# Performance work log

Measured on AMD Instinct MI355X. Metric: run time of the kernel, lower is better.

Reference implementation:

```python
import jax, jax.numpy as jnp
import numpy as np
import math

D = 2048
H = 8
DK = D // H // 2  # 128
NL = 3
EPS = 1e-6
SCALE = 1.0 / math.sqrt(DK)


def _ln(x, g, b):
    m = jnp.mean(x, axis=-1, keepdims=True)
    v = jnp.mean(jnp.square(x - m), axis=-1, keepdims=True)
    return (x - m) * jax.lax.rsqrt(v + EPS) * g + b


def _attn_layer(x, g, b, Wq, Wk, Wv):
    bs = x.shape[0]
    xn = _ln(x, g, b)
    # torch Linear: y = x @ W.T ; reshape to (bs, h, 2, d_k)
    q = (xn @ Wq.T).reshape(bs, H, 2, DK)
    k = (xn @ Wk.T).reshape(bs, H, 2, DK)
    v = (xn @ Wv.T).reshape(bs, H, 2, DK)
    s = jnp.einsum('bhpd,bhqd->bhpq', q, k) * SCALE  # tiny 2x2 scores
    a = jax.nn.softmax(s, axis=-1)
    o = jnp.einsum('bhpq,bhqd->bhpd', a, v).reshape(bs, D)
    return o + x


def _ff_layer(x, lnd_g, lnd_b, lnt_g, lnt_b, Wd1, bd1, Wd2, bd2, Wt1, bt1, Wt2, bt2):
    d, t = x[:, :D // 2], x[:, D // 2:]
    dn = _ln(d, lnd_g, lnd_b)
    tn = _ln(t, lnt_g, lnt_b)
    do = jax.nn.relu(dn @ Wd1.T + bd1) @ Wd2.T + bd2
    to = jax.nn.relu(tn @ Wt1.T + bt1) @ Wt2.T + bt2
    return jnp.concatenate([do, to], axis=-1) + x


def setup_inputs() -> dict:
    key = jax.random.key(0)
    ks = iter(jax.random.split(key, 64))
    s = 0.02
    inp = {}
    inp['x'] = jax.random.normal(next(ks), (8192, D), dtype=jnp.float32)
    # attention stacks: NL layers
    inp['attn_ln_g'] = jnp.ones((NL, D), jnp.float32)
    inp['attn_ln_b'] = jnp.zeros((NL, D), jnp.float32)
    inp['Wq'] = jax.random.normal(next(ks), (NL, D, D), jnp.float32) * s
    inp['Wk'] = jax.random.normal(next(ks), (NL, D, D), jnp.float32) * s
    inp['Wv'] = jax.random.normal(next(ks), (NL, D, D), jnp.float32) * s
    # feedforward stacks: NL-1 layers
    F = NL - 1
    hd = D // 2
    inp['ff_lnd_g'] = jnp.ones((F, hd), jnp.float32)
    inp['ff_lnd_b'] = jnp.zeros((F, hd), jnp.float32)
    inp['ff_lnt_g'] = jnp.ones((F, hd), jnp.float32)
    inp['ff_lnt_b'] = jnp.zeros((F, hd), jnp.float32)
    inp['Wd1'] = jax.random.normal(next(ks), (F, D, hd), jnp.float32) * s
    inp['bd1'] = jnp.zeros((F, D), jnp.float32)
    inp['Wd2'] = jax.random.normal(next(ks), (F, hd, D), jnp.float32) * s
    inp['bd2'] = jnp.zeros((F, hd), jnp.float32)
    inp['Wt1'] = jax.random.normal(next(ks), (F, D, hd), jnp.float32) * s
    inp['bt1'] = jnp.zeros((F, D), jnp.float32)
    inp['Wt2'] = jax.random.normal(next(ks), (F, hd, D), jnp.float32) * s
    inp['bt2'] = jnp.zeros((F, hd), jnp.float32)
    # output head
    inp['Wo1'] = jax.random.normal(next(ks), (hd, D), jnp.float32) * s
    inp['bo1'] = jnp.zeros((hd,), jnp.float32)
    inp['Wo2'] = jax.random.normal(next(ks), (1, hd), jnp.float32) * s
    inp['bo2'] = jnp.zeros((1,), jnp.float32)
    return inp


def reference(x, attn_ln_g, attn_ln_b, Wq, Wk, Wv,
              ff_lnd_g, ff_lnd_b, ff_lnt_g, ff_lnt_b,
              Wd1, bd1, Wd2, bd2, Wt1, bt1, Wt2, bt2,
              Wo1, bo1, Wo2, bo2):
    for n in range(NL - 1):
        x = _attn_layer(x, attn_ln_g[n], attn_ln_b[n], Wq[n], Wk[n], Wv[n])
        x = _ff_layer(x, ff_lnd_g[n], ff_lnd_b[n], ff_lnt_g[n], ff_lnt_b[n],
                      Wd1[n], bd1[n], Wd2[n], bd2[n], Wt1[n], bt1[n], Wt2[n], bt2[n])
    x = _attn_layer(x, attn_ln_g[-1], attn_ln_b[-1], Wq[-1], Wk[-1], Wv[-1])
    h = jax.nn.relu(x @ Wo1.T + bo1)
    return h @ Wo2.T + bo2  # [bs, 1]
```

## Files before the change

### kernel.cpp

```cpp
#include <hip/hip_runtime.h>
#include <stdint.h>


typedef __bf16 bf16x8 __attribute__((ext_vector_type(8)));
typedef float f32x4 __attribute__((ext_vector_type(4)));

static __device__ __forceinline__ float bf2f(unsigned short u) {
  unsigned int x = ((unsigned int)u) << 16;
  float f;
  __builtin_memcpy(&f, &x, 4);
  return f;
}
static __device__ __forceinline__ unsigned short f2bf(float f) {
  unsigned int x;
  __builtin_memcpy(&x, &f, 4);
  x += 0x7fffu + ((x >> 16) & 1u);
  return (unsigned short)(x >> 16);
}

static __device__ __forceinline__ void gload_lds16(const void* g, void* l) {
  __builtin_amdgcn_global_load_lds(
      (const __attribute__((address_space(1))) unsigned int*)g,
      (__attribute__((address_space(3))) unsigned int*)l, 16, 0, 0);
}

__global__ __launch_bounds__(256) void cvt_kernel(
    const float* __restrict__ in, unsigned short* __restrict__ out, long n) {
  const long i = ((long)blockIdx.x * 256 + threadIdx.x) * 4;
  if (i + 3 < n) {
    float4 f = *(const float4*)(in + i);
    *(ushort4*)(out + i) = make_ushort4(f2bf(f.x), f2bf(f.y), f2bf(f.z), f2bf(f.w));
  }
}

#define BARRIER __builtin_amdgcn_s_barrier()
#define LGKM(N)                                                     \
  do {                                                              \
    asm volatile("s_waitcnt lgkmcnt(" #N ")" ::: "memory");         \
    __builtin_amdgcn_sched_barrier(0);                              \
  } while (0)
#define VMC(N)                                                      \
  do {                                                              \
    asm volatile("s_waitcnt vmcnt(" #N ")" ::: "memory");           \
    __builtin_amdgcn_sched_barrier(0);                              \
  } while (0)

__global__ __launch_bounds__(512, 2) void gemm8_kernel(
    const unsigned short* __restrict__ A, int lda,
    const unsigned short* __restrict__ B, int K,
    void* __restrict__ Cp, int ldc, const float* __restrict__ bias,
    int relu, int out_f32, int resadd,
    const unsigned short* __restrict__ A2, const unsigned short* __restrict__ B2,
    void* __restrict__ C2p, const float* __restrict__ bias2, int dual) {
  extern __shared__ __align__(16) char smem[];

  const int tid = threadIdx.x;
  const int lane = tid & 63;
  const int w = tid >> 6;
  const int wm = w >> 2;
  const int wn = w & 3;
  const long brow = (long)blockIdx.y * 256;

  const unsigned short* Ap = A;
  const unsigned short* Bp = B;
  const float* bi = bias;
  void* Cq = Cp;
  long bcol;
  if (dual && (int)blockIdx.x >= (int)(gridDim.x >> 1)) {
    Ap = A2; Bp = B2; bi = bias2; Cq = C2p;
    bcol = (long)(blockIdx.x - (gridDim.x >> 1)) * 256;
  } else {
    bcol = (long)blockIdx.x * 256;
  }

  const int NT = K >> 6;

  const int lrA = tid >> 3;
  const int scb = ((tid & 7) * 16) ^ (((tid >> 3) & 7) << 4);
  const unsigned wb = (unsigned)(tid & ~63) * 16;
  const long ldab = (long)lda * 2;
  const long ldbb = (long)K * 2;
  const char* gA = (const char*)Ap + (brow + lrA) * ldab + scb;
  const char* gB = (const char*)Bp + (bcol + lrA) * ldbb + scb;
  const long a64 = 64 * ldab, a128 = 128 * ldab, a192 = 192 * ldab;
  const long b64 = 64 * ldbb, b128 = 128 * ldbb, b192 = 192 * ldbb;

#define STAGE_A(bb, off)                                        \
  do {                                                          \
    gload_lds16(gA + (off), smem + (bb) + wb);                  \
    gload_lds16(gA + a64 + (off), smem + (bb) + 8192 + wb);     \
    gload_lds16(gA + a128 + (off), smem + (bb) + 16384 + wb);   \
    gload_lds16(gA + a192 + (off), smem + (bb) + 24576 + wb);   \
  } while (0)
#define STAGE_B(bb, off)                                        \
  do {                                                          \
    gload_lds16(gB + (off), smem + (bb) + 32768 + wb);          \
    gload_lds16(gB + b64 + (off), smem + (bb) + 40960 + wb);    \
    gload_lds16(gB + b128 + (off), smem + (bb) + 49152 + wb);   \
    gload_lds16(gB + b192 + (off), smem + (bb) + 57344 + wb);   \
  } while (0)

  f32x4 acc[8][4];
  const f32x4 fz = {0.f, 0.f, 0.f, 0.f};
#pragma unroll
  for (int m = 0; m < 8; ++m)
#pragma unroll
    for (int n = 0; n < 4; ++n) acc[m][n] = fz;

  const int frow = lane & 15;
  const int fkb = (lane >> 4) * 16;
  const int fswz = (lane & 7) << 4;

#define RDA(dst, CB, M, KK)                                                   \
  dst = *(const bf16x8*)(smem + (CB) + (wm * 128 + (M) * 16 + frow) * 128 +   \
                         (((KK) * 64 + fkb) ^ fswz))
#define RDB(dst, CB, N, KK)                                                   \
  dst = *(const bf16x8*)(smem + (CB) + 32768 +                                \
                         (wn * 64 + (N) * 16 + frow) * 128 +                  \
                         (((KK) * 64 + fkb) ^ fswz))

#define MM8(AF, MA, BF, NA, MO, NO)                                           \
  do {                                                                        \
    _Pragma("unroll") for (int kk = 0; kk < 2; ++kk)                          \
    _Pragma("unroll") for (int mm = 0; mm < 2; ++mm)                          \
    _Pragma("unroll") for (int nn = 0; nn < 2; ++nn)                          \
        acc[(MO) + mm][(NO) + nn] = __builtin_amdgcn_mfma_f32_16x16x32_bf16(  \
            AF[(MA) + mm][kk], BF[(NA) + nn][kk], acc[(MO) + mm][(NO) + nn],  \
            0, 0, 0);                                                         \
  } while (0)
#define MM8N(AF, BF, NB, NO)                                                  \
  do {                                                                        \
    _Pragma("unroll") for (int kk = 0; kk < 2; ++kk)                          \
    _Pragma("unroll") for (int mm = 0; mm < 4; ++mm)                          \
        acc[mm][(NO)] = __builtin_amdgcn_mfma_f32_16x16x32_bf16(              \
            AF[mm][kk], BF[(NB)][kk], acc[mm][(NO)], 0, 0, 0);                \
  } while (0)

  bf16x8 afL[4][2], afH[4][2], bfvL[2][2], bfvH[2][2];

  STAGE_A(0, 0);
  STAGE_B(0, 0);
  STAGE_A(65536, 128);
  STAGE_B(65536, 128);
  VMC(8);
  BARRIER;
  long soff = 256;

#define TILE_IT(T, CB)                                                        \
  do {                                                                        \
                                       \
    RDB(bfvL[0][0], CB, 0, 0); RDB(bfvL[0][1], CB, 0, 1);                     \
    RDB(bfvL[1][0], CB, 1, 0); RDB(bfvL[1][1], CB, 1, 1);                     \
    RDA(afL[0][0], CB, 0, 0); RDA(afL[0][1], CB, 0, 1);                       \
    RDA(afL[1][0], CB, 1, 0); RDA(afL[1][1], CB, 1, 1);                       \
    RDA(afL[2][0], CB, 2, 0); RDA(afL[2][1], CB, 2, 1);                       \
    RDA(afL[3][0], CB, 3, 0); RDA(afL[3][1], CB, 3, 1);                       \
    BARRIER;                                                                  \
    LGKM(4);                                                                  \
    __builtin_amdgcn_s_setprio(1);                                            \
    MM8(afL, 0, bfvL, 0, 0, 0);                                               \
    LGKM(0);                                                                  \
    MM8(afL, 2, bfvL, 0, 2, 0);                                               \
    __builtin_amdgcn_s_setprio(0);                                            \
    BARRIER;                                                                  \
                                              \
    RDB(bfvH[0][0], CB, 2, 0); RDB(bfvH[0][1], CB, 2, 1);                     \
    RDB(bfvH[1][0], CB, 3, 0); RDB(bfvH[1][1], CB, 3, 1);                     \
    BARRIER;                                                                  \
    LGKM(2);                                                                  \
    __builtin_amdgcn_s_setprio(1);                                            \
    MM8N(afL, bfvH, 0, 2);                                                    \
    LGKM(0);                                                                  \
    MM8N(afL, bfvH, 1, 3);                                                    \
    __builtin_amdgcn_s_setprio(0);                                            \
    BARRIER;                                                                  \
                                \
    RDA(afH[0][0], CB, 4, 0); RDA(afH[0][1], CB, 4, 1);                       \
    RDA(afH[1][0], CB, 5, 0); RDA(afH[1][1], CB, 5, 1);                       \
    RDA(afH[2][0], CB, 6, 0); RDA(afH[2][1], CB, 6, 1);                       \
    RDA(afH[3][0], CB, 7, 0); RDA(afH[3][1], CB, 7, 1);                       \
    if ((T) + 2 < NT) STAGE_B(CB, soff);                                      \
    BARRIER;                                                                  \
    LGKM(4);                                                                  \
    __builtin_amdgcn_s_setprio(1);                                            \
    MM8(afH, 0, bfvL, 0, 4, 0);                                               \
    LGKM(0);                                                                  \
    MM8(afH, 2, bfvL, 0, 6, 0);                                               \
    __builtin_amdgcn_s_setprio(0);                                            \
    BARRIER;                                                                  \
                                \
    if ((T) + 2 < NT) {                                                       \
      STAGE_A(CB, soff);                                                      \
      VMC(8);                                                                 \
    } else {                                                                  \
      VMC(0);                                                                 \
    }                                                                         \
    BARRIER;                                                                  \
    __builtin_amdgcn_s_setprio(1);                                            \
    MM8(afH, 0, bfvH, 0, 4, 2);                                               \
    MM8(afH, 2, bfvH, 0, 6, 2);                                               \
    __builtin_amdgcn_s_setprio(0);                                            \
    BARRIER;                                                                  \
    soff += 128;                                                              \
  } while (0)

  for (int t = 0; t < NT; t += 2) {
    TILE_IT(t, 0);
    TILE_IT(t + 1, 65536);
  }

  const long rb0 = brow + wm * 128 + (lane >> 4) * 4;
  const long cb0 = bcol + wn * 64 + (lane & 15);
#pragma unroll
  for (int m = 0; m < 8; ++m) {
#pragma unroll
    for (int n = 0; n < 4; ++n) {
      const long col = cb0 + n * 16;
      const float bv = bi ? bi[col] : 0.f;
#pragma unroll
      for (int j = 0; j < 4; ++j) {
        const long r = rb0 + m * 16 + j;
        float v = acc[m][n][j] + bv;
        if (relu) v = fmaxf(v, 0.f);
        if (out_f32) {
          float* cp = (float*)Cq + r * (long)ldc + col;
          if (resadd) v += *cp;
          *cp = v;
        } else {
          ((unsigned short*)Cq)[r * (long)ldc + col] = f2bf(v);
        }
      }
    }
  }
#undef TILE_IT
#undef STAGE_A
#undef STAGE_B
#undef RDA
#undef RDB
#undef MM8
#undef MM8N
}

__global__ __launch_bounds__(256) void gemm_bt_kernel(
    const unsigned short* __restrict__ A, int lda,
    const unsigned short* __restrict__ B, int K,
    void* __restrict__ Cp, int ldc,
    const float* __restrict__ bias,
    const void* __restrict__ res, int res_mode, int ldres,
    int relu, int out_f32) {
  __shared__ __align__(16) unsigned short As[128 * 32];
  __shared__ __align__(16) unsigned short Bs[128 * 32];

  const int t = threadIdx.x;
  const int lane = t & 63;
  const int w = t >> 6;
  const int wr = (w >> 1) * 64;
  const int wc = (w & 1) * 64;
  const long brow = (long)blockIdx.y * 128;
  const long bcol = (long)blockIdx.x * 128;

  const int srow = lane >> 2;
  const int scol = (lane & 3) * 8;
  const unsigned short* Ab = A + (brow + w * 32 + srow) * (long)lda + scol;
  const unsigned short* Bb = B + (bcol + w * 32 + srow) * (long)K + scol;
  unsigned short* Asb = &As[(w * 32) * 32];
  unsigned short* Bsb = &Bs[(w * 32) * 32];

  f32x4 acc[4][4];
  const f32x4 fzero = {0.f, 0.f, 0.f, 0.f};
#pragma unroll
  for (int m = 0; m < 4; ++m)
#pragma unroll
    for (int n = 0; n < 4; ++n) acc[m][n] = fzero;

  const int fr = lane & 15;
  const int fk = (lane >> 4) * 8;

  for (int kt = 0; kt < K; kt += 32) {
    gload_lds16(Ab + kt, Asb);
    gload_lds16(Ab + 16 * (long)lda + kt, Asb + 16 * 32);
    gload_lds16(Bb + kt, Bsb);
    gload_lds16(Bb + 16 * (long)K + kt, Bsb + 16 * 32);
    __syncthreads();

    bf16x8 af[4], bfv[4];
#pragma unroll
    for (int m = 0; m < 4; ++m)
      af[m] = *(const bf16x8*)&As[(wr + m * 16 + fr) * 32 + fk];
#pragma unroll
    for (int n = 0; n < 4; ++n)
      bfv[n] = *(const bf16x8*)&Bs[(wc + n * 16 + fr) * 32 + fk];
#pragma unroll
    for (int m = 0; m < 4; ++m)
#pragma unroll
      for (int n = 0; n < 4; ++n)
        acc[m][n] = __builtin_amdgcn_mfma_f32_16x16x32_bf16(af[m], bfv[n],
                                                            acc[m][n], 0, 0, 0);
    __syncthreads();
  }

  const long rbase = brow + wr + (lane >> 4) * 4;
#pragma unroll
  for (int m = 0; m < 4; ++m) {
#pragma unroll
    for (int n = 0; n < 4; ++n) {
      const long col = bcol + wc + n * 16 + fr;
      const float bv = bias ? bias[col] : 0.f;
#pragma unroll
      for (int j = 0; j < 4; ++j) {
        const long r = rbase + m * 16 + j;
        float v = acc[m][n][j] + bv;
        if (relu) v = fmaxf(v, 0.f);
        if (res_mode == 1)
          v += ((const float*)res)[r * (long)ldres + col];
        else if (res_mode == 2)
          v += bf2f(((const unsigned short*)res)[r * (long)ldres + col]);
        if (out_f32)
          ((float*)Cp)[r * (long)ldc + col] = v;
        else
          ((unsigned short*)Cp)[r * (long)ldc + col] = f2bf(v);
      }
    }
  }
}

template <int L>
__global__ __launch_bounds__(256) void ln_kernel(
    const void* __restrict__ inp, int in_bf16, int ldin,
    const float* __restrict__ g, const float* __restrict__ b,
    unsigned short* __restrict__ outp, int ldout) {
  constexpr int VEC = L / 256;
  const long row = blockIdx.x;
  const int t = threadIdx.x;
  float v[VEC];
  if (in_bf16) {
    const unsigned short* p = (const unsigned short*)inp + row * (long)ldin + t * VEC;
#pragma unroll
    for (int i = 0; i < VEC; i += 4) {
      ushort4 u = *(const ushort4*)(p + i);
      v[i] = bf2f(u.x); v[i + 1] = bf2f(u.y); v[i + 2] = bf2f(u.z); v[i + 3] = bf2f(u.w);
    }
  } else {
    const float* p = (const float*)inp + row * (long)ldin + t * VEC;
#pragma unroll
    for (int i = 0; i < VEC; i += 4) {
      float4 f = *(const float4*)(p + i);
      v[i] = f.x; v[i + 1] = f.y; v[i + 2] = f.z; v[i + 3] = f.w;
    }
  }
  float s = 0.f, sq = 0.f;
#pragma unroll
  for (int i = 0; i < VEC; ++i) { s += v[i]; sq += v[i] * v[i]; }
#pragma unroll
  for (int off = 32; off; off >>= 1) {
    s += __shfl_xor(s, off, 64);
    sq += __shfl_xor(sq, off, 64);
  }
  __shared__ float red[8];
  if ((t & 63) == 0) { red[t >> 6] = s; red[4 + (t >> 6)] = sq; }
  __syncthreads();
  s = red[0] + red[1] + red[2] + red[3];
  sq = red[4] + red[5] + red[6] + red[7];
  const float mean = s * (1.f / L);
  const float var = sq * (1.f / L) - mean * mean;
  const float rstd = rsqrtf(var + 1e-6f);
  unsigned short* op = outp + row * (long)ldout + t * VEC;
  const float* gp = g + t * VEC;
  const float* bp = b + t * VEC;
#pragma unroll
  for (int i = 0; i < VEC; i += 4) {
    float4 gg = *(const float4*)(gp + i);
    float4 bb = *(const float4*)(bp + i);
    *(ushort4*)(op + i) = make_ushort4(
        f2bf((v[i + 0] - mean) * rstd * gg.x + bb.x),
        f2bf((v[i + 1] - mean) * rstd * gg.y + bb.y),
        f2bf((v[i + 2] - mean) * rstd * gg.z + bb.z),
        f2bf((v[i + 3] - mean) * rstd * gg.w + bb.w));
  }
}

__global__ __launch_bounds__(512) void attn_glue_kernel(
    const unsigned short* __restrict__ Q, const unsigned short* __restrict__ Kq,
    const unsigned short* __restrict__ V, int ld, const void* __restrict__ Xres,
    int res_bf16, void* __restrict__ Xout, int out_bf16,
    unsigned short* __restrict__ Xout_bf,
    unsigned short* __restrict__ DNp, unsigned short* __restrict__ TNp,
    const float* __restrict__ lnd_g, const float* __restrict__ lnd_b,
    const float* __restrict__ lnt_g, const float* __restrict__ lnt_b) {
  const long row = blockIdx.x;
  const int h = threadIdx.x >> 6;
  const int lane = threadIdx.x & 63;
  const long qbase = row * (long)ld + h * 256;
  const long xbase = row * 2048 + h * 256;
  const int d = lane * 2;

  ushort2 q0 = *(const ushort2*)&Q[qbase + d];
  ushort2 q1 = *(const ushort2*)&Q[qbase + 128 + d];
  ushort2 k0 = *(const ushort2*)&Kq[qbase + d];
  ushort2 k1 = *(const ushort2*)&Kq[qbase + 128 + d];
  ushort2 v0 = *(const ushort2*)&V[qbase + d];
  ushort2 v1 = *(const ushort2*)&V[qbase + 128 + d];

  const float q0x = bf2f(q0.x), q0y = bf2f(q0.y);
  const float q1x = bf2f(q1.x), q1y = bf2f(q1.y);
  const float k0x = bf2f(k0.x), k0y = bf2f(k0.y);
  const float k1x = bf2f(k1.x), k1y = bf2f(k1.y);

  float s00 = q0x * k0x + q0y * k0y;
  float s01 = q0x * k1x + q0y * k1y;
  float s10 = q1x * k0x + q1y * k0y;
  float s11 = q1x * k1x + q1y * k1y;
#pragma unroll
  for (int off = 32; off; off >>= 1) {
    s00 += __shfl_xor(s00, off, 64);
    s01 += __shfl_xor(s01, off, 64);
    s10 += __shfl_xor(s10, off, 64);
    s11 += __shfl_xor(s11, off, 64);
  }
  const float SC = 0.088388347648318447f;
  s00 *= SC; s01 *= SC; s10 *= SC; s11 *= SC;
  const float m0 = fmaxf(s00, s01), m1 = fmaxf(s10, s11);
  const float e00 = __expf(s00 - m0), e01 = __expf(s01 - m0);
  const float e10 = __expf(s10 - m1), e11 = __expf(s11 - m1);
  const float i0 = 1.f / (e00 + e01), i1 = 1.f / (e10 + e11);
  const float a00 = e00 * i0, a01 = e01 * i0;
  const float a10 = e10 * i1, a11 = e11 * i1;

  const float v0x = bf2f(v0.x), v0y = bf2f(v0.y);
  const float v1x = bf2f(v1.x), v1y = bf2f(v1.y);
  float o0x = a00 * v0x + a01 * v1x, o0y = a00 * v0y + a01 * v1y;
  float o1x = a10 * v0x + a11 * v1x, o1y = a10 * v0y + a11 * v1y;

  if (res_bf16) {
    const unsigned short* xr = (const unsigned short*)Xres + xbase;
    ushort2 ra = *(const ushort2*)&xr[d];
    ushort2 rb = *(const ushort2*)&xr[128 + d];
    o0x += bf2f(ra.x); o0y += bf2f(ra.y); o1x += bf2f(rb.x); o1y += bf2f(rb.y);
  } else {
    const float* xr = (const float*)Xres + xbase;
    float2 ra = *(const float2*)&xr[d];
    float2 rb = *(const float2*)&xr[128 + d];
    o0x += ra.x; o0y += ra.y; o1x += rb.x; o1y += rb.y;
  }
  if (out_bf16) {
    unsigned short* xo = (unsigned short*)Xout + xbase;
    *(ushort2*)&xo[d] = make_ushort2(f2bf(o0x), f2bf(o0y));
    *(ushort2*)&xo[128 + d] = make_ushort2(f2bf(o1x), f2bf(o1y));
  } else {
    float* xo = (float*)Xout + xbase;
    *(float2*)&xo[d] = make_float2(o0x, o0y);
    *(float2*)&xo[128 + d] = make_float2(o1x, o1y);
  }
  if (Xout_bf) {
    unsigned short* xb = Xout_bf + xbase;
    *(ushort2*)&xb[d] = make_ushort2(f2bf(o0x), f2bf(o0y));
    *(ushort2*)&xb[128 + d] = make_ushort2(f2bf(o1x), f2bf(o1y));
  }

  if (DNp) {
    float s4 = o0x + o0y + o1x + o1y;
    float q4 = o0x * o0x + o0y * o0y + o1x * o1x + o1y * o1y;
#pragma unroll
    for (int off = 32; off; off >>= 1) {
      s4 += __shfl_xor(s4, off, 64);
      q4 += __shfl_xor(q4, off, 64);
    }
    __shared__ float redS[8], redQ[8];
    if (lane == 0) { redS[h] = s4; redQ[h] = q4; }
    __syncthreads();
    const int b4 = (h >> 2) * 4;
    const float S = redS[b4] + redS[b4 + 1] + redS[b4 + 2] + redS[b4 + 3];
    const float Qs = redQ[b4] + redQ[b4 + 1] + redQ[b4 + 2] + redQ[b4 + 3];
    const float mean = S * (1.f / 1024.f);
    const float var = Qs * (1.f / 1024.f) - mean * mean;
    const float rstd = rsqrtf(var + 1e-6f);
    const float* gp = (h < 4) ? lnd_g : lnt_g;
    const float* bp = (h < 4) ? lnd_b : lnt_b;
    unsigned short* dst = ((h < 4) ? DNp : TNp) + row * 1024;
    const int hc = (h & 3) * 256 + d;
    float2 g0 = *(const float2*)&gp[hc];
    float2 b0 = *(const float2*)&bp[hc];
    *(ushort2*)&dst[hc] = make_ushort2(f2bf((o0x - mean) * rstd * g0.x + b0.x),
                                       f2bf((o0y - mean) * rstd * g0.y + b0.y));
    float2 g1 = *(const float2*)&gp[hc + 128];
    float2 b1 = *(const float2*)&bp[hc + 128];
    *(ushort2*)&dst[hc + 128] =
        make_ushort2(f2bf((o1x - mean) * rstd * g1.x + b1.x),
                     f2bf((o1y - mean) * rstd * g1.y + b1.y));
  }
}

__global__ __launch_bounds__(256) void final_matvec_kernel(
    const unsigned short* __restrict__ Hm, const float* __restrict__ wv,
    const float* __restrict__ b2, float* __restrict__ outp) {
  const long row = blockIdx.x;
  const int t = threadIdx.x;
  ushort4 hv = *(const ushort4*)&Hm[row * 1024 + t * 4];
  float4 wq = *(const float4*)&wv[t * 4];
  float s = bf2f(hv.x) * wq.x + bf2f(hv.y) * wq.y +
            bf2f(hv.z) * wq.z + bf2f(hv.w) * wq.w;
#pragma unroll
  for (int off = 32; off; off >>= 1) s += __shfl_xor(s, off, 64);
  __shared__ float red[4];
  if ((t & 63) == 0) red[t >> 6] = s;
  __syncthreads();
  if (t == 0) outp[row] = red[0] + red[1] + red[2] + red[3] + b2[0];
}

extern "C" void kernel_launch(void* const* d_in, const int* in_sizes, int n_in,
                              void* d_out, int out_size, void* d_ws,
                              size_t ws_size, hipStream_t stream) {
  const float* x_in = (const float*)d_in[0];
  const float* aln_g = (const float*)d_in[1];
  const float* aln_b = (const float*)d_in[2];
  const float* Wq_f = (const float*)d_in[3];
  const float* Wk_f = (const float*)d_in[4];
  const float* Wv_f = (const float*)d_in[5];
  const float* lnd_g = (const float*)d_in[6];
  const float* lnd_b = (const float*)d_in[7];
  const float* lnt_g = (const float*)d_in[8];
  const float* lnt_b = (const float*)d_in[9];
  const float* Wd1_f = (const float*)d_in[10];
  const float* bd1 = (const float*)d_in[11];
  const float* Wd2_f = (const float*)d_in[12];
  const float* bd2 = (const float*)d_in[13];
  const float* Wt1_f = (const float*)d_in[14];
  const float* bt1 = (const float*)d_in[15];
  const float* Wt2_f = (const float*)d_in[16];
  const float* bt2 = (const float*)d_in[17];
  const float* Wo1_f = (const float*)d_in[18];
  const float* bo1 = (const float*)d_in[19];
  const float* Wo2_f = (const float*)d_in[20];
  const float* bo2 = (const float*)d_in[21];

  const size_t R = 8192, D = 2048, HD = 1024;
  const size_t DD = D * D;
  const size_t WALL = (3 * 3 * DD + 4 * 2 * D * HD + HD * D) * 2;
  const size_t SLOT = 3 * DD * 2;
  const size_t ACT = R * D * 4 + R * D * 2 + R * 6144 * 2;

  auto cvt = [&](const float* src, unsigned short* dst, long n) {
    cvt_kernel<<<dim3((unsigned)(n / 1024)), dim3(256), 0, stream>>>(src, dst, n);
  };

  if (ws_size >= ACT + SLOT) {
    const bool planAll = ws_size >= ACT + WALL;
    hipFuncSetAttribute(reinterpret_cast<const void*>(gemm8_kernel),
                        hipFuncAttributeMaxDynamicSharedMemorySize, 131072);

    char* p = (char*)d_ws;
    float* Xf = (float*)p; p += R * D * 4;
    unsigned short* XN = (unsigned short*)p; p += R * D * 2;
    unsigned short* QKVb = (unsigned short*)p; p += R * 6144 * 2;
    unsigned short* Warea = (unsigned short*)p;

    unsigned short* H1d = QKVb;
    unsigned short* H1t = QKVb + R * 2048;
    unsigned short* Hfin = QKVb + R * 4096;
    unsigned short* DN = XN;
    unsigned short* TN = XN + R * HD;

    unsigned short* Wqkv_b = Warea;
    unsigned short* Wd1_b = Wqkv_b + 9 * DD;
    unsigned short* Wt1_b = Wd1_b + 2 * D * HD;
    unsigned short* Wd2_b = Wt1_b + 2 * D * HD;
    unsigned short* Wt2_b = Wd2_b + 2 * D * HD;
    unsigned short* Wo1_b = Wt2_b + 2 * D * HD;
    if (planAll) {
      for (int n = 0; n < 3; ++n) {
        cvt(Wq_f + n * DD, Wqkv_b + n * 3 * DD + 0 * DD, DD);
        cvt(Wk_f + n * DD, Wqkv_b + n * 3 * DD + 1 * DD, DD);
        cvt(Wv_f + n * DD, Wqkv_b + n * 3 * DD + 2 * DD, DD);
      }
      cvt(Wd1_f, Wd1_b, 2 * D * HD);
      cvt(Wt1_f, Wt1_b, 2 * D * HD);
      cvt(Wd2_f, Wd2_b, 2 * D * HD);
      cvt(Wt2_f, Wt2_b, 2 * D * HD);
      cvt(Wo1_f, Wo1_b, HD * D);
    }

    auto gemm8 = [&](const unsigned short* A, int lda, const unsigned short* B,
                     int N, int K, void* C, int ldc, const float* bias,
                     int relu, int of32, int resadd, const unsigned short* A2,
                     const unsigned short* B2, void* C2, const float* bias2) {
      const int dual = (A2 != nullptr);
      dim3 grid((dual ? 2 : 1) * (N / 256), 32);
      gemm8_kernel<<<grid, dim3(512), 131072, stream>>>(
          A, lda, B, K, C, ldc, bias, relu, of32, resadd, A2, B2, C2, bias2,
          dual);
    };

    for (int n = 0; n < 3; ++n) {
      ln_kernel<2048><<<8192, 256, 0, stream>>>(
          (n == 0) ? (const void*)x_in : (const void*)Xf, 0, 2048,
          aln_g + n * D, aln_b + n * D, XN, 2048);
      const unsigned short* Wqkv;
      if (planAll) {
        Wqkv = Wqkv_b + (size_t)n * 3 * DD;
      } else {
        cvt(Wq_f + n * DD, Warea + 0 * DD, DD);
        cvt(Wk_f + n * DD, Warea + 1 * DD, DD);
        cvt(Wv_f + n * DD, Warea + 2 * DD, DD);
        Wqkv = Warea;
      }
      gemm8(XN, 2048, Wqkv, 6144, 2048, QKVb, 6144, nullptr, 0, 0, 0,
            nullptr, nullptr, nullptr, nullptr);
      attn_glue_kernel<<<8192, 512, 0, stream>>>(
          QKVb, QKVb + 2048, QKVb + 4096, 6144,
          (n == 0) ? (const void*)x_in : (const void*)Xf, 0, Xf, 0,
          (n == 2) ? XN : nullptr,
          (n < 2) ? DN : nullptr, (n < 2) ? TN : nullptr,
          (n < 2) ? lnd_g + n * HD : nullptr, (n < 2) ? lnd_b + n * HD : nullptr,
          (n < 2) ? lnt_g + n * HD : nullptr, (n < 2) ? lnt_b + n * HD : nullptr);

      if (n < 2) {
        const size_t fo = (size_t)n * D * HD;
        const unsigned short *w1d, *w1t, *w2d, *w2t;
        if (planAll) {
          w1d = Wd1_b + fo; w1t = Wt1_b + fo; w2d = Wd2_b + fo; w2t = Wt2_b + fo;
        } else {
          cvt(Wd1_f + fo, Warea + 0 * D * HD, D * HD);
          cvt(Wt1_f + fo, Warea + 1 * D * HD, D * HD);
          cvt(Wd2_f + fo, Warea + 2 * D * HD, D * HD);
          cvt(Wt2_f + fo, Warea + 3 * D * HD, D * HD);
          w1d = Warea; w1t = Warea + D * HD; w2d = Warea + 2 * D * HD;
          w2t = Warea + 3 * D * HD;
        }
        gemm8(DN, 1024, w1d, 2048, 1024, H1d, 2048, bd1 + n * D, 1, 0, 0,
              TN, w1t, H1t, bt1 + n * D);
        gemm8(H1d, 2048, w2d, 1024, 2048, Xf, 2048, bd2 + n * HD, 0, 1, 1,
              H1t, w2t, Xf + HD, bt2 + n * HD);
      }
    }

    const unsigned short* Wo1p;
    if (planAll) {
      Wo1p = Wo1_b;
    } else {
      cvt(Wo1_f, Warea, HD * D);
      Wo1p = Warea;
    }
    gemm8(XN, 2048, Wo1p, 1024, 2048, Hfin, 1024, bo1, 1, 0, 0,
          nullptr, nullptr, nullptr, nullptr);
    final_matvec_kernel<<<8192, 256, 0, stream>>>(Hfin, Wo2_f, bo2,
                                                  (float*)d_out);
    return;
  }

  const size_t PLB = R * D * 2;
  const size_t XFZ = R * D * 4;
  const size_t SLOT1 = DD * 2;
  const bool planAll = ws_size >= XFZ + 4 * PLB + WALL;
  const bool xIsF32 = planAll || ws_size >= XFZ + 4 * PLB + SLOT1;

  char* p = (char*)d_ws;
  float* Xf = nullptr;
  unsigned short* Xb = nullptr;
  if (xIsF32) { Xf = (float*)p; p += XFZ; } else { Xb = (unsigned short*)p; p += PLB; }
  unsigned short* XN = (unsigned short*)p; p += PLB;
  unsigned short* Qb = (unsigned short*)p; p += PLB;
  unsigned short* Kb = (unsigned short*)p; p += PLB;
  unsigned short* Vb = (unsigned short*)p; p += PLB;
  unsigned short* Warea = (unsigned short*)p;

  void* X = xIsF32 ? (void*)Xf : (void*)Xb;
  const int xres_mode = xIsF32 ? 1 : 2;
  unsigned short* H1 = Qb;
  unsigned short* DN = XN;
  unsigned short* TN = XN + R * HD;
  unsigned short* Hfin = Vb;

  unsigned short* Wq_b = Warea;
  unsigned short* Wk_b = Wq_b + 3 * DD;
  unsigned short* Wv_b = Wk_b + 3 * DD;
  unsigned short* Wd1_b = Wv_b + 3 * DD;
  unsigned short* Wd2_b = Wd1_b + 2 * D * HD;
  unsigned short* Wt1_b = Wd2_b + 2 * D * HD;
  unsigned short* Wt2_b = Wt1_b + 2 * D * HD;
  unsigned short* Wo1_b = Wt2_b + 2 * D * HD;
  if (planAll) {
    cvt(Wq_f, Wq_b, 3 * DD);
    cvt(Wk_f, Wk_b, 3 * DD);
    cvt(Wv_f, Wv_b, 3 * DD);
    cvt(Wd1_f, Wd1_b, 2 * D * HD);
    cvt(Wd2_f, Wd2_b, 2 * D * HD);
    cvt(Wt1_f, Wt1_b, 2 * D * HD);
    cvt(Wt2_f, Wt2_b, 2 * D * HD);
    cvt(Wo1_f, Wo1_b, HD * D);
  }
  auto wbf = [&](const float* src_base, unsigned short* pre_base, size_t off,
                 size_t cnt) -> const unsigned short* {
    if (planAll) return pre_base + off;
    cvt(src_base + off, Warea, (long)cnt);
    return Warea;
  };
  auto gemm = [&](const unsigned short* A, int lda, const unsigned short* B,
                  int N, int K, void* C, int ldc, const float* bias,
                  const void* res, int res_mode, int ldres, int relu, int of32) {
    dim3 grid(N / 128, 8192 / 128);
    gemm_bt_kernel<<<grid, dim3(256), 0, stream>>>(
        A, lda, B, K, C, ldc, bias, res, res_mode, ldres, relu, of32);
  };

  for (int n = 0; n < 3; ++n) {
    const void* lin = (n == 0) ? (const void*)x_in : (const void*)X;
    const int lin_bf16 = (n == 0) ? 0 : (xIsF32 ? 0 : 1);
    ln_kernel<2048><<<8192, 256, 0, stream>>>(lin, lin_bf16, 2048,
                                              aln_g + n * D, aln_b + n * D, XN, 2048);
    const size_t wo = (size_t)n * DD;
    gemm(XN, 2048, wbf(Wq_f, Wq_b, wo, DD), 2048, 2048, Qb, 2048,
         nullptr, nullptr, 0, 0, 0, 0);
    gemm(XN, 2048, wbf(Wk_f, Wk_b, wo, DD), 2048, 2048, Kb, 2048,
         nullptr, nullptr, 0, 0, 0, 0);
    gemm(XN, 2048, wbf(Wv_f, Wv_b, wo, DD), 2048, 2048, Vb, 2048,
         nullptr, nullptr, 0, 0, 0, 0);
    attn_glue_kernel<<<8192, 512, 0, stream>>>(
        Qb, Kb, Vb, 2048, (n == 0) ? (const void*)x_in : (const void*)X,
        (n == 0) ? 0 : (xIsF32 ? 0 : 1), X, xIsF32 ? 0 : 1,
        (n == 2 && xIsF32) ? XN : nullptr,
        nullptr, nullptr, nullptr, nullptr, nullptr, nullptr);

    if (n < 2) {
      const size_t fo = (size_t)n * D * HD;
      ln_kernel<1024><<<8192, 256, 0, stream>>>(X, !xIsF32, 2048,
                                                lnd_g + n * HD, lnd_b + n * HD, DN, 1024);
      const void* Xt = xIsF32 ? (const void*)(Xf + HD) : (const void*)(Xb + HD);
      ln_kernel<1024><<<8192, 256, 0, stream>>>(Xt, !xIsF32, 2048,
                                                lnt_g + n * HD, lnt_b + n * HD, TN, 1024);
      void* Xd2 = X;
      void* Xt2 = xIsF32 ? (void*)(Xf + HD) : (void*)(Xb + HD);
      gemm(DN, 1024, wbf(Wd1_f, Wd1_b, fo, D * HD), 2048, 1024, H1, 2048,
           bd1 + n * D, nullptr, 0, 0, 1, 0);
      gemm(H1, 2048, wbf(Wd2_f, Wd2_b, fo, D * HD), 1024, 2048, Xd2, 2048,
           bd2 + n * HD, Xd2, xres_mode, 2048, 0, xIsF32 ? 1 : 0);
      gemm(TN, 1024, wbf(Wt1_f, Wt1_b, fo, D * HD), 2048, 1024, H1, 2048,
           bt1 + n * D, nullptr, 0, 0, 1, 0);
      gemm(H1, 2048, wbf(Wt2_f, Wt2_b, fo, D * HD), 1024, 2048, Xt2, 2048,
           bt2 + n * HD, Xt2, xres_mode, 2048, 0, xIsF32 ? 1 : 0);
    }
  }

  const unsigned short* Afin = xIsF32 ? XN : Xb;
  gemm(Afin, 2048, wbf(Wo1_f, Wo1_b, 0, HD * D), 1024, 2048, Hfin, 1024,
       bo1, nullptr, 0, 0, 1, 0);
  final_matvec_kernel<<<8192, 256, 0, stream>>>(Hfin, Wo2_f, bo2, (float*)d_out);
}
```

Measured before the change: 1.323 ms.

## Remap GEMM workgroups per XCD, batch weight casts, simplify LDS waits, skip dead store

The GEMM kernel now remaps block IDs so each XCD gets a contiguous chunk of output tiles, aiming to improve L2 reuse of A/B panels. The fourteen separate weight-conversion launches are merged into one multi-segment cast kernel to cut launch overhead. The LDS wait counts in the main loop are simplified to full waits before the MFMA groups, which gives up some overlap between LDS reads and math. The last attention layer also skips writing the fp32 residual output, since only the bf16 copy is consumed afterwards.

```diff
diff --git a/kernel.cpp b/kernel.cpp
--- a/kernel.cpp
+++ b/kernel.cpp
@@ -31,6 +31,23 @@
     float4 f = *(const float4*)(in + i);
     *(ushort4*)(out + i) = make_ushort4(f2bf(f.x), f2bf(f.y), f2bf(f.z), f2bf(f.w));
   }
+}
+
+#define MAXSEG 14
+struct CvtArgs {
+  const float* src[MAXSEG];
+  unsigned short* dst[MAXSEG];
+  long pfx[MAXSEG + 1];
+  int ns;
+};
+__global__ __launch_bounds__(256) void cvt_multi_kernel(CvtArgs a) {
+  const long i = ((long)blockIdx.x * 256 + threadIdx.x) * 4;
+  int s = 0;
+  while (s + 1 < a.ns && i >= a.pfx[s + 1]) ++s;
+  const long off = i - a.pfx[s];
+  float4 f = *(const float4*)(a.src[s] + off);
+  *(ushort4*)(a.dst[s] + off) =
+      make_ushort4(f2bf(f.x), f2bf(f.y), f2bf(f.z), f2bf(f.w));
 }
 
 #define BARRIER __builtin_amdgcn_s_barrier()
@@ -59,18 +76,27 @@
   const int w = tid >> 6;
   const int wm = w >> 2;
   const int wn = w & 3;
-  const long brow = (long)blockIdx.y * 256;
+
+  const int gx = (int)gridDim.x;
+  const int nwg = gx * (int)gridDim.y;
+  const int orig = (int)blockIdx.y * gx + (int)blockIdx.x;
+  const int qch = nwg >> 3, rch = nwg & 7, xcd = orig & 7, io = orig >> 3;
+  const int wgid =
+      (xcd < rch ? xcd * (qch + 1) : rch * (qch + 1) + (xcd - rch) * qch) + io;
+  const int bx = wgid % gx;
+  const int by = wgid / gx;
+  const long brow = (long)by * 256;
 
   const unsigned short* Ap = A;
   const unsigned short* Bp = B;
   const float* bi = bias;
   void* Cq = Cp;
   long bcol;
-  if (dual && (int)blockIdx.x >= (int)(gridDim.x >> 1)) {
+  if (dual && bx >= (gx >> 1)) {
     Ap = A2; Bp = B2; bi = bias2; Cq = C2p;
-    bcol = (long)(blockIdx.x - (gridDim.x >> 1)) * 256;
+    bcol = (long)(bx - (gx >> 1)) * 256;
   } else {
-    bcol = (long)blockIdx.x * 256;
+    bcol = (long)bx * 256;
   }
 
   const int NT = K >> 6;
@@ -148,18 +174,18 @@
 
 #define TILE_IT(T, CB)                                                        \
   do {                                                                        \
-                                       \
+                            \
     RDB(bfvL[0][0], CB, 0, 0); RDB(bfvL[0][1], CB, 0, 1);                     \
     RDB(bfvL[1][0], CB, 1, 0); RDB(bfvL[1][1], CB, 1, 1);                     \
     RDA(afL[0][0], CB, 0, 0); RDA(afL[0][1], CB, 0, 1);                       \
     RDA(afL[1][0], CB, 1, 0); RDA(afL[1][1], CB, 1, 1);                       \
     RDA(afL[2][0], CB, 2, 0); RDA(afL[2][1], CB, 2, 1);                       \
     RDA(afL[3][0], CB, 3, 0); RDA(afL[3][1], CB, 3, 1);                       \
+    LGKM(8);                    \
     BARRIER;                                                                  \
-    LGKM(4);                                                                  \
+    LGKM(0);                                                                  \
     __builtin_amdgcn_s_setprio(1);                                            \
     MM8(afL, 0, bfvL, 0, 0, 0);                                               \
-    LGKM(0);                                                                  \
     MM8(afL, 2, bfvL, 0, 2, 0);                                               \
     __builtin_amdgcn_s_setprio(0);                                            \
     BARRIER;                                                                  \
@@ -167,13 +193,13 @@
     RDB(bfvH[0][0], CB, 2, 0); RDB(bfvH[0][1], CB, 2, 1);                     \
     RDB(bfvH[1][0], CB, 3, 0); RDB(bfvH[1][1], CB, 3, 1);                     \
     BARRIER;                                                                  \
-    LGKM(2);                                                                  \
+    LGKM(0);                                                                  \
     __builtin_amdgcn_s_setprio(1);                                            \
     MM8N(afL, bfvH, 0, 2);                                                    \
-    LGKM(0);                                                                  \
     MM8N(afL, bfvH, 1, 3);                                                    \
     __builtin_amdgcn_s_setprio(0);                                            \
     BARRIER;                                                                  \
+                 \
                                 \
     RDA(afH[0][0], CB, 4, 0); RDA(afH[0][1], CB, 4, 1);                       \
     RDA(afH[1][0], CB, 5, 0); RDA(afH[1][1], CB, 5, 1);                       \
@@ -181,19 +207,19 @@
     RDA(afH[3][0], CB, 7, 0); RDA(afH[3][1], CB, 7, 1);                       \
     if ((T) + 2 < NT) STAGE_B(CB, soff);                                      \
     BARRIER;                                                                  \
-    LGKM(4);                                                                  \
+    LGKM(0);                                                                  \
     __builtin_amdgcn_s_setprio(1);                                            \
     MM8(afH, 0, bfvL, 0, 4, 0);                                               \
-    LGKM(0);                                                                  \
     MM8(afH, 2, bfvL, 0, 6, 0);                                               \
     __builtin_amdgcn_s_setprio(0);                                            \
     BARRIER;                                                                  \
+                 \
                                 \
     if ((T) + 2 < NT) {                                                       \
       STAGE_A(CB, soff);                                                      \
-      VMC(8);                                                                 \
+      VMC(8);                                      \
     } else {                                                                  \
-      VMC(0);                                                                 \
+      VMC(0);                                                 \
     }                                                                         \
     BARRIER;                                                                  \
     __builtin_amdgcn_s_setprio(1);                                            \
@@ -442,14 +468,16 @@
     float2 rb = *(const float2*)&xr[128 + d];
     o0x += ra.x; o0y += ra.y; o1x += rb.x; o1y += rb.y;
   }
-  if (out_bf16) {
-    unsigned short* xo = (unsigned short*)Xout + xbase;
-    *(ushort2*)&xo[d] = make_ushort2(f2bf(o0x), f2bf(o0y));
-    *(ushort2*)&xo[128 + d] = make_ushort2(f2bf(o1x), f2bf(o1y));
-  } else {
-    float* xo = (float*)Xout + xbase;
-    *(float2*)&xo[d] = make_float2(o0x, o0y);
-    *(float2*)&xo[128 + d] = make_float2(o1x, o1y);
+  if (Xout) {
+    if (out_bf16) {
+      unsigned short* xo = (unsigned short*)Xout + xbase;
+      *(ushort2*)&xo[d] = make_ushort2(f2bf(o0x), f2bf(o0y));
+      *(ushort2*)&xo[128 + d] = make_ushort2(f2bf(o1x), f2bf(o1y));
+    } else {
+      float* xo = (float*)Xout + xbase;
+      *(float2*)&xo[d] = make_float2(o0x, o0y);
+      *(float2*)&xo[128 + d] = make_float2(o1x, o1y);
+    }
   }
   if (Xout_bf) {
     unsigned short* xb = Xout_bf + xbase;
@@ -567,16 +595,25 @@
     unsigned short* Wt2_b = Wd2_b + 2 * D * HD;
     unsigned short* Wo1_b = Wt2_b + 2 * D * HD;
     if (planAll) {
+      CvtArgs ca;
+      int s = 0;
+      long pfx = 0;
+      auto add = [&](const float* src, unsigned short* dst, long n) {
+        ca.src[s] = src; ca.dst[s] = dst; ca.pfx[s] = pfx; pfx += n; ++s;
+      };
       for (int n = 0; n < 3; ++n) {
-        cvt(Wq_f + n * DD, Wqkv_b + n * 3 * DD + 0 * DD, DD);
-        cvt(Wk_f + n * DD, Wqkv_b + n * 3 * DD + 1 * DD, DD);
-        cvt(Wv_f + n * DD, Wqkv_b + n * 3 * DD + 2 * DD, DD);
+        add(Wq_f + n * DD, Wqkv_b + n * 3 * DD + 0 * DD, (long)DD);
+        add(Wk_f + n * DD, Wqkv_b + n * 3 * DD + 1 * DD, (long)DD);
+        add(Wv_f + n * DD, Wqkv_b + n * 3 * DD + 2 * DD, (long)DD);
       }
-      cvt(Wd1_f, Wd1_b, 2 * D * HD);
-      cvt(Wt1_f, Wt1_b, 2 * D * HD);
-      cvt(Wd2_f, Wd2_b, 2 * D * HD);
-      cvt(Wt2_f, Wt2_b, 2 * D * HD);
-      cvt(Wo1_f, Wo1_b, HD * D);
+      add(Wd1_f, Wd1_b, (long)(2 * D * HD));
+      add(Wt1_f, Wt1_b, (long)(2 * D * HD));
+      add(Wd2_f, Wd2_b, (long)(2 * D * HD));
+      add(Wt2_f, Wt2_b, (long)(2 * D * HD));
+      add(Wo1_f, Wo1_b, (long)(HD * D));
+      ca.pfx[s] = pfx;
+      ca.ns = s;
+      cvt_multi_kernel<<<dim3((unsigned)(pfx / 1024)), dim3(256), 0, stream>>>(ca);
     }
 
     auto gemm8 = [&](const unsigned short* A, int lda, const unsigned short* B,
@@ -607,7 +644,8 @@
             nullptr, nullptr, nullptr, nullptr);
       attn_glue_kernel<<<8192, 512, 0, stream>>>(
           QKVb, QKVb + 2048, QKVb + 4096, 6144,
-          (n == 0) ? (const void*)x_in : (const void*)Xf, 0, Xf, 0,
+          (n == 0) ? (const void*)x_in : (const void*)Xf, 0,
+          (n < 2) ? (void*)Xf : nullptr, 0,
           (n == 2) ? XN : nullptr,
           (n < 2) ? DN : nullptr, (n < 2) ? TN : nullptr,
           (n < 2) ? lnd_g + n * HD : nullptr, (n < 2) ? lnd_b + n * HD : nullptr,
```

Result: no change. 1.322 ms (-0.0%).
